# Kernel tuning notes

Measured on AMD Instinct MI355X. Metric: run time of the kernel, lower is better.

Reference implementation:

```python
import jax, jax.numpy as jnp
import numpy as np

IN_FEATURES = 4096
OUT_FEATURES = 4096


def fht(x):
    """Normalized fast Walsh-Hadamard transform along last axis (n = power of 2).
    Equals x @ H_n / sqrt(n); matches matmul_hadU(t)_cuda when had_K is None (K=1)."""
    n = x.shape[-1]
    orig_shape = x.shape
    x = x.reshape(-1, n)
    h = 1
    while h < n:
        x = x.reshape(-1, n // (2 * h), 2, h)
        a = x[:, :, 0, :]
        b = x[:, :, 1, :]
        x = jnp.stack([a + b, a - b], axis=2).reshape(-1, n)
        h *= 2
    scale = jnp.asarray(1.0 / np.sqrt(n), dtype=x.dtype)
    return (x * scale).reshape(orig_shape)


def decode_e8p(Qidxs, grid_abs):
    """E8P12-style decode: each 16-bit codeword -> 8 fp16 weights.
    Low 8 bits index a 256-entry table of 8 absolute values; high 8 bits are
    per-element sign flips. Returns dense W of shape [out, in]."""
    idx = Qidxs.astype(jnp.int32) & 0xFFFF            # [out, in/8]
    abs_vals = grid_abs[idx & 0xFF]                   # [out, in/8, 8]
    sbits = (idx[..., None] >> (8 + jnp.arange(8, dtype=jnp.int32))) & 1
    signs = (1 - 2 * sbits).astype(grid_abs.dtype)    # [out, in/8, 8] in {+1,-1}
    w = abs_vals * signs
    return w.reshape(Qidxs.shape[0], -1)              # [out, in]


def setup_inputs() -> dict:
    key = jax.random.key(0)
    k1, k2, k3, k4, k5, k6 = jax.random.split(key, 6)
    inp = {}
    inp["input"] = jax.random.normal(k1, (2, 4096, IN_FEATURES), dtype=jnp.float16)
    inp["Qidxs"] = jax.random.randint(k2, (OUT_FEATURES, IN_FEATURES // 8), 0, 65536, dtype=jnp.int32)
    # abs half-integer-ish grid values (E8 lattice magnitudes live in ~[0.25, 3.75])
    inp["grid_abs"] = (jax.random.uniform(k3, (256, 8), dtype=jnp.float32) * 3.0 + 0.25).astype(jnp.float16)
    # SU/SV are random sign vectors in QuIP
    inp["SU"] = (1 - 2 * jax.random.bernoulli(k4, 0.5, (IN_FEATURES,)).astype(jnp.float16))
    inp["SV"] = (1 - 2 * jax.random.bernoulli(k5, 0.5, (OUT_FEATURES,)).astype(jnp.float16))
    inp["Wscale"] = jnp.ones((), dtype=jnp.float32)
    inp["bias"] = jax.random.normal(k6, (OUT_FEATURES,), dtype=jnp.float16) * jnp.float16(0.01)
    return inp


def reference(input, Qidxs, grid_abs, SU, SV, Wscale, bias):
    x = input.reshape(-1, input.shape[-1])            # [T, in]
    x = x * SU                                        # input sign rescale
    x = fht(x)                                        # H^T x / sqrt(n) (H symmetric)
    x = (x * Wscale).astype(jnp.float16)              # global weight scale
    W = decode_e8p(Qidxs, grid_abs)                   # [out, in] dequantized lattice weights
    out = jnp.dot(x, W.T, preferred_element_type=jnp.float32).astype(jnp.float16)  # [T, out]
    out = fht(out)                                    # output Hadamard
    out = out * SV + bias                             # output sign rescale + bias
    return out.reshape(*input.shape[:-1], out.shape[-1])
```

## Files before the change

kernel.cpp:

```cpp
#include <hip/hip_runtime.h>
#include <hip/hip_bf16.h>
#include <stdint.h>

typedef _Float16 f16;
typedef _Float16 f16x8 __attribute__((ext_vector_type(8)));
typedef float f32x4 __attribute__((ext_vector_type(4)));

#define N_FEAT 4096
#define M_ROWS 8192
#define QSTRIDE 512

#define GLD16(gptr, lptr)                                                      \
  __builtin_amdgcn_global_load_lds(                                            \
      (const __attribute__((address_space(1))) void*)(gptr),                   \
      (__attribute__((address_space(3))) void*)(uint32_t)(uintptr_t)(lptr),    \
      16, 0, 0)

#define PAD64(i) ((i) + (((i) >> 6) << 2))

__device__ __forceinline__ void fht16(float v[16]) {
#pragma unroll
  for (int h = 1; h < 16; h <<= 1) {
#pragma unroll
    for (int i = 0; i < 16; i += (h << 1)) {
#pragma unroll
      for (int j = 0; j < h; ++j) {
        float a = v[i + j], b = v[i + j + h];
        v[i + j] = a + b;
        v[i + j + h] = a - b;
      }
    }
  }
}

__device__ __forceinline__ void fht4(float& a, float& b, float& c, float& d) {
  float t0 = a + b, t1 = a - b, t2 = c + d, t3 = c - d;
  a = t0 + t2; b = t1 + t3; c = t0 - t2; d = t1 - t3;
}

__global__ __launch_bounds__(256) void k_fht_in(const float* __restrict__ x,
                                                const float* __restrict__ SU,
                                                const float* __restrict__ wscale,
                                                f16* __restrict__ out) {
  __shared__ float lds[4096 + 256];
  const int row = blockIdx.x;
  const int t = threadIdx.x;
  const float* xr = x + (size_t)row * N_FEAT;
  float v[16];

#pragma unroll
  for (int j = 0; j < 4; ++j) {
    const float4 a = *(const float4*)(xr + (t << 4) + 4 * j);
    const float4 s = *(const float4*)(SU + (t << 4) + 4 * j);
    v[4 * j + 0] = a.x * s.x; v[4 * j + 1] = a.y * s.y;
    v[4 * j + 2] = a.z * s.z; v[4 * j + 3] = a.w * s.w;
  }
  fht16(v);
#pragma unroll
  for (int j = 0; j < 4; ++j)
    *(float4*)&lds[PAD64((t << 4) + 4 * j)] =
        make_float4(v[4 * j], v[4 * j + 1], v[4 * j + 2], v[4 * j + 3]);
  __syncthreads();

  const int a = t & 15, b = t >> 4;
#pragma unroll
  for (int j = 0; j < 16; ++j) v[j] = lds[PAD64((b << 8) + (j << 4) + a)];
  fht16(v);
#pragma unroll
  for (int j = 0; j < 16; ++j) lds[PAD64((b << 8) + (j << 4) + a)] = v[j];
  __syncthreads();

#pragma unroll
  for (int j = 0; j < 16; ++j) v[j] = lds[PAD64((j << 8) + t)];
  fht16(v);
  const float s = wscale[0] * 0.015625f;
  f16* op = out + (size_t)row * N_FEAT;
#pragma unroll
  for (int j = 0; j < 16; ++j) op[(j << 8) + t] = (f16)(v[j] * s);
}

__global__ __launch_bounds__(256) void k_wA(const int* __restrict__ q,
                                            const float* __restrict__ grid,
                                            f16* __restrict__ Wp) {
  __shared__ float tabf[2048];
  __shared__ float tile[64 * 65];
  const int t = threadIdx.x;
  const int kg = blockIdx.x;
  const int ng = blockIdx.y;
  {
    *(float4*)&tabf[t * 8] = *(const float4*)(grid + t * 8);
    *(float4*)&tabf[t * 8 + 4] = *(const float4*)(grid + t * 8 + 4);
  }
  __syncthreads();

#pragma unroll
  for (int e2 = 0; e2 < 2; ++e2) {
    const int e = t + (e2 << 8);
    const int nl = e >> 3, c = e & 7;
    const unsigned code =
        (unsigned)q[(size_t)(ng * 64 + nl) * QSTRIDE + kg * 8 + c] & 0xffffu;
    const float* tb = &tabf[(code & 255u) * 8];
#pragma unroll
    for (int j = 0; j < 8; ++j) {
      const int bi = __float_as_int(tb[j]) ^ (int)(((code >> (8 + j)) & 1u) << 31);
      tile[nl * 65 + (c << 3) + j] = __int_as_float(bi);
    }
  }
  __syncthreads();

  {
    const int k = t & 63, p = t >> 6;
    float v[16];
#pragma unroll
    for (int j = 0; j < 16; ++j) v[j] = tile[(16 * p + j) * 65 + k];
    fht16(v);
#pragma unroll
    for (int j = 0; j < 16; ++j) tile[(16 * p + j) * 65 + k] = v[j];
  }
  __syncthreads();

  {
    const int k = t & 63, base = (t >> 6) << 2;
#pragma unroll
    for (int bb = 0; bb < 4; ++bb) {
      const int low = base + bb;
      float v0 = tile[(low) * 65 + k],      v1 = tile[(low + 16) * 65 + k];
      float v2 = tile[(low + 32) * 65 + k], v3 = tile[(low + 48) * 65 + k];
      fht4(v0, v1, v2, v3);
      tile[(low) * 65 + k] = v0;      tile[(low + 16) * 65 + k] = v1;
      tile[(low + 32) * 65 + k] = v2; tile[(low + 48) * 65 + k] = v3;
    }
  }
  __syncthreads();

  {
    const int nl = t >> 2, koff = (t & 3) << 4;
    union { f16 h[16]; int4 v[2]; } u;
#pragma unroll
    for (int i = 0; i < 16; ++i) u.h[i] = (f16)tile[nl * 65 + koff + i];
    int4* dst = (int4*)(Wp + (size_t)(ng * 64 + nl) * N_FEAT + kg * 64 + koff);
    dst[0] = u.v[0];
    dst[1] = u.v[1];
  }
}

__global__ __launch_bounds__(256) void k_wB(f16* __restrict__ Wp) {
  __shared__ float tile[64 * 65];
  const int t = threadIdx.x;
  const int kg = blockIdx.x;
  const int n0 = blockIdx.y;
  {
    const int n1 = t >> 2, koff = (t & 3) << 4;
    const f16* src = Wp + (size_t)(n0 + 64 * n1) * N_FEAT + kg * 64 + koff;
    union { f16 h[16]; int4 v[2]; } u;
    u.v[0] = ((const int4*)src)[0];
    u.v[1] = ((const int4*)src)[1];
#pragma unroll
    for (int i = 0; i < 16; ++i) tile[n1 * 65 + koff + i] = (float)u.h[i];
  }
  __syncthreads();
  {
    const int k = t & 63, p = t >> 6;
    float v[16];
#pragma unroll
    for (int j = 0; j < 16; ++j) v[j] = tile[(16 * p + j) * 65 + k];
    fht16(v);
#pragma unroll
    for (int j = 0; j < 16; ++j) tile[(16 * p + j) * 65 + k] = v[j];
  }
  __syncthreads();
  {
    const int k = t & 63, base = (t >> 6) << 2;
#pragma unroll
    for (int bb = 0; bb < 4; ++bb) {
      const int low = base + bb;
      float v0 = tile[(low) * 65 + k],      v1 = tile[(low + 16) * 65 + k];
      float v2 = tile[(low + 32) * 65 + k], v3 = tile[(low + 48) * 65 + k];
      fht4(v0, v1, v2, v3);
      tile[(low) * 65 + k] = v0;      tile[(low + 16) * 65 + k] = v1;
      tile[(low + 32) * 65 + k] = v2; tile[(low + 48) * 65 + k] = v3;
    }
  }
  __syncthreads();
  {
    const int n1 = t >> 2, koff = (t & 3) << 4;
    union { f16 h[16]; int4 v[2]; } u;
#pragma unroll
    for (int i = 0; i < 16; ++i) u.h[i] = (f16)tile[n1 * 65 + koff + i];
    int4* dst = (int4*)(Wp + (size_t)(n0 + 64 * n1) * N_FEAT + kg * 64 + koff);
    dst[0] = u.v[0];
    dst[1] = u.v[1];
  }
}

#define BM 256
#define BN 256
#define BK 64
#define KDIM 4096

#define WAITB(n)                                          \
  asm volatile("s_waitcnt vmcnt(" #n ")" ::: "memory");   \
  __builtin_amdgcn_s_barrier();

#define SCHED_FENCE() __builtin_amdgcn_sched_barrier(0)

#define STAGE_HALF(gbase, lhalf)                                         \
  {                                                                      \
    _Pragma("unroll")                                                    \
    for (int i_ = 0; i_ < 2; ++i_) {                                     \
      const int rb_ = (w << 4) + (i_ << 3);                              \
      const int r_ = rb_ + srow;                                         \
      const int kc_ = scc ^ (r_ & 7);                                    \
      GLD16((gbase) + (size_t)r_ * KDIM + (kc_ << 3), (lhalf) + (rb_ << 6)); \
    }                                                                    \
  }

#define LDA(dst, mh)                                                     \
  {                                                                      \
    _Pragma("unroll")                                                    \
    for (int i_ = 0; i_ < 4; ++i_) {                                     \
      const int m_ = ((mh) << 7) + (wr << 6) + (i_ << 4) + ml;           \
      _Pragma("unroll")                                                  \
      for (int s_ = 0; s_ < 2; ++s_) {                                   \
        const int kc_ = ((s_ << 2) + quad) ^ (m_ & 7);                   \
        dst[i_][s_] = *(const f16x8*)&sA[cur][(m_ << 6) + (kc_ << 3)];   \
      }                                                                  \
    }                                                                    \
  }

#define LDB(dst, nh)                                                     \
  {                                                                      \
    _Pragma("unroll")                                                    \
    for (int j_ = 0; j_ < 2; ++j_) {                                     \
      const int n_ = ((nh) << 7) + (wc << 5) + (j_ << 4) + ml;           \
      _Pragma("unroll")                                                  \
      for (int s_ = 0; s_ < 2; ++s_) {                                   \
        const int kc_ = ((s_ << 2) + quad) ^ (n_ & 7);                   \
        dst[j_][s_] = *(const f16x8*)&sB[cur][(n_ << 6) + (kc_ << 3)];   \
      }                                                                  \
    }                                                                    \
  }

#define MMAQ(mh, nh)                                                     \
  {                                                                      \
    __builtin_amdgcn_s_setprio(1);                                       \
    _Pragma("unroll")                                                    \
    for (int i_ = 0; i_ < 4; ++i_) {                                     \
      _Pragma("unroll")                                                  \
      for (int j_ = 0; j_ < 2; ++j_) {                                   \
        acc[(mh) * 4 + i_][(nh) * 2 + j_] =                              \
            __builtin_amdgcn_mfma_f32_16x16x32_f16(                      \
                af[i_][0], bf[j_][0], acc[(mh) * 4 + i_][(nh) * 2 + j_], \
                0, 0, 0);                                                \
        acc[(mh) * 4 + i_][(nh) * 2 + j_] =                              \
            __builtin_amdgcn_mfma_f32_16x16x32_f16(                      \
                af[i_][1], bf[j_][1], acc[(mh) * 4 + i_][(nh) * 2 + j_], \
                0, 0, 0);                                                \
      }                                                                  \
    }                                                                    \
    __builtin_amdgcn_s_setprio(0);                                       \
  }

__global__ __launch_bounds__(512, 2) void k_gemm(const f16* __restrict__ A,
                                                 const f16* __restrict__ B,
                                                 float* __restrict__ C,
                                                 const float* __restrict__ SV,
                                                 const float* __restrict__ bias) {
  __shared__ __attribute__((aligned(16))) f16 sA[2][BM * BK];
  __shared__ __attribute__((aligned(16))) f16 sB[2][BN * BK];

  const int tid = threadIdx.x;
  const int lane = tid & 63;
  const int w = tid >> 6;
  const int wr = w >> 2;
  const int wc = w & 3;

  const int lin = blockIdx.y * gridDim.x + blockIdx.x;
  const int swz = ((lin & 7) << 6) | (lin >> 3);
  const int m0 = (swz >> 4) * BM;
  const int n0 = (swz & 15) * BN;

  const int quad = lane >> 4;
  const int ml = lane & 15;
  const int srow = lane >> 3;
  const int scc = lane & 7;

  f32x4 acc[8][4];
#pragma unroll
  for (int i = 0; i < 8; ++i)
#pragma unroll
    for (int j = 0; j < 4; ++j) acc[i][j] = (f32x4)0.0f;

  const f16* Ab = A + (size_t)m0 * KDIM;
  const f16* Bb = B + (size_t)n0 * KDIM;

  STAGE_HALF(Ab, &sA[0][0]);
  SCHED_FENCE();
  STAGE_HALF(Bb, &sB[0][0]);
  SCHED_FENCE();
  STAGE_HALF(Bb + (size_t)128 * KDIM, &sB[0][128 * 64]);
  SCHED_FENCE();
  STAGE_HALF(Ab + (size_t)128 * KDIM, &sA[0][128 * 64]);
  WAITB(4);

  f16x8 af[4][2], bf[2][2];

#pragma unroll 2
  for (int t = 0; t < 64; ++t) {
    const int cur = t & 1;
    const int nxt = cur ^ 1;
    const int kn = ((t + 1) & 63) << 6;
    const f16* An = Ab + kn;
    const f16* Bn = Bb + kn;

    STAGE_HALF(An, &sA[nxt][0]);
    LDA(af, 0);
    LDB(bf, 0);
    MMAQ(0, 0);

    WAITB(4);
    STAGE_HALF(Bn, &sB[nxt][0]);
    LDB(bf, 1);
    MMAQ(0, 1);

    WAITB(4);
    STAGE_HALF(Bn + (size_t)128 * KDIM, &sB[nxt][128 * 64]);
    LDA(af, 1);
    MMAQ(1, 1);

    SCHED_FENCE();
    STAGE_HALF(An + (size_t)128 * KDIM, &sA[nxt][128 * 64]);
    LDB(bf, 0);
    MMAQ(1, 0);
    WAITB(4);
  }

  asm volatile("s_waitcnt vmcnt(0)" ::: "memory");

#pragma unroll
  for (int nj = 0; nj < 4; ++nj) {
    const int col = n0 + ((nj >> 1) << 7) + (wc << 5) + ((nj & 1) << 4) + ml;
    const float sv = SV[col] * 0.015625f;
    const float bs = bias[col];
#pragma unroll
    for (int mi = 0; mi < 8; ++mi) {
      const int rowb =
          m0 + ((mi >> 2) << 7) + (wr << 6) + ((mi & 3) << 4) + (quad << 2);
#pragma unroll
      for (int r = 0; r < 4; ++r)
        C[(size_t)(rowb + r) * N_FEAT + col] = acc[mi][nj][r] * sv + bs;
    }
  }
}

extern "C" void kernel_launch(void* const* d_in, const int* in_sizes, int n_in,
                              void* d_out, int out_size, void* d_ws, size_t ws_size,
                              hipStream_t stream) {
  const float* input = nullptr;
  const int* qidxs = nullptr;
  const float* grid_abs = nullptr;
  const float* wscale = nullptr;
  const float* v4k[3] = {nullptr, nullptr, nullptr};
  int n4 = 0;
  for (int i = 0; i < n_in; ++i) {
    switch (in_sizes[i]) {
      case 33554432: input = (const float*)d_in[i]; break;
      case 2097152:  qidxs = (const int*)d_in[i]; break;
      case 2048:     grid_abs = (const float*)d_in[i]; break;
      case 1:        wscale = (const float*)d_in[i]; break;
      case 4096:     if (n4 < 3) v4k[n4++] = (const float*)d_in[i]; break;
      default: break;
    }
  }
  const float* SU = v4k[0];
  const float* SV = v4k[1];
  const float* bias = v4k[2];

  f16* x = (f16*)d_ws;
  f16* Wp;
  if (ws_size >= (size_t)100663296) {
    Wp = (f16*)((char*)d_ws + 67108864);
  } else {
    Wp = (f16*)const_cast<float*>(input);
  }
  float* out = (float*)d_out;

  k_fht_in<<<M_ROWS, 256, 0, stream>>>(input, SU, wscale, x);
  dim3 gw(64, 64);
  k_wA<<<gw, 256, 0, stream>>>(qidxs, grid_abs, Wp);
  k_wB<<<gw, 256, 0, stream>>>(Wp);
  dim3 g(N_FEAT / BN, M_ROWS / BM);
  k_gemm<<<g, 512, 0, stream>>>(x, Wp, out, SV, bias);
}
```

Baseline: 486.8 us.

## Restructure input FHT to one wavefront per row and keep both B fragments

The input Hadamard kernel now handles four rows per block, one wavefront per row, using an XOR-swizzled LDS layout and float4-vectorised LDS accesses in the second and third butterfly stages. Outputs are written as packed 4-wide f16 stores. In the GEMM, the low and high B fragments are held in separate registers, so the final quadrant reuses the low fragment instead of reloading it from LDS. This removes LDS traffic and bank conflicts at the cost of more VGPRs in the GEMM and larger LDS use per block in the FHT kernel.

```diff
diff --git a/kernel.cpp b/kernel.cpp
--- a/kernel.cpp
+++ b/kernel.cpp
@@ -33,50 +33,92 @@
   }
 }
 
+__device__ __forceinline__ void fht16v(f32x4 v[16]) {
+#pragma unroll
+  for (int h = 1; h < 16; h <<= 1) {
+#pragma unroll
+    for (int i = 0; i < 16; i += (h << 1)) {
+#pragma unroll
+      for (int j = 0; j < h; ++j) {
+        f32x4 a = v[i + j], b = v[i + j + h];
+        v[i + j] = a + b;
+        v[i + j + h] = a - b;
+      }
+    }
+  }
+}
+
 __device__ __forceinline__ void fht4(float& a, float& b, float& c, float& d) {
   float t0 = a + b, t1 = a - b, t2 = c + d, t3 = c - d;
   a = t0 + t2; b = t1 + t3; c = t0 - t2; d = t1 - t3;
 }
+
+#define SWZ(c) ((c) ^ (((((c) >> 4) ^ ((c) >> 8)) & 7) << 2))
 
 __global__ __launch_bounds__(256) void k_fht_in(const float* __restrict__ x,
                                                 const float* __restrict__ SU,
                                                 const float* __restrict__ wscale,
                                                 f16* __restrict__ out) {
-  __shared__ float lds[4096 + 256];
-  const int row = blockIdx.x;
+  __shared__ __attribute__((aligned(16))) float lds[4 * 4096];
   const int t = threadIdx.x;
-  const float* xr = x + (size_t)row * N_FEAT;
-  float v[16];
-
-#pragma unroll
-  for (int j = 0; j < 4; ++j) {
-    const float4 a = *(const float4*)(xr + (t << 4) + 4 * j);
-    const float4 s = *(const float4*)(SU + (t << 4) + 4 * j);
-    v[4 * j + 0] = a.x * s.x; v[4 * j + 1] = a.y * s.y;
-    v[4 * j + 2] = a.z * s.z; v[4 * j + 3] = a.w * s.w;
-  }
-  fht16(v);
-#pragma unroll
-  for (int j = 0; j < 4; ++j)
-    *(float4*)&lds[PAD64((t << 4) + 4 * j)] =
-        make_float4(v[4 * j], v[4 * j + 1], v[4 * j + 2], v[4 * j + 3]);
-  __syncthreads();
-
-  const int a = t & 15, b = t >> 4;
-#pragma unroll
-  for (int j = 0; j < 16; ++j) v[j] = lds[PAD64((b << 8) + (j << 4) + a)];
-  fht16(v);
-#pragma unroll
-  for (int j = 0; j < 16; ++j) lds[PAD64((b << 8) + (j << 4) + a)] = v[j];
-  __syncthreads();
-
-#pragma unroll
-  for (int j = 0; j < 16; ++j) v[j] = lds[PAD64((j << 8) + t)];
-  fht16(v);
-  const float s = wscale[0] * 0.015625f;
-  f16* op = out + (size_t)row * N_FEAT;
-#pragma unroll
-  for (int j = 0; j < 16; ++j) op[(j << 8) + t] = (f16)(v[j] * s);
+  const int rw = t >> 6;
+  const int u = t & 63;
+  const size_t row = (size_t)blockIdx.x * 4 + rw;
+  float* pl = &lds[rw << 12];
+  const float* xr = x + row * N_FEAT;
+
+#pragma unroll
+  for (int g = 0; g < 4; ++g) {
+    const int c16 = (g << 10) + (u << 4);
+    float v[16];
+#pragma unroll
+    for (int q = 0; q < 4; ++q) {
+      const f32x4 a = *(const f32x4*)(xr + c16 + (q << 2));
+      const f32x4 s4 = *(const f32x4*)(SU + c16 + (q << 2));
+      const f32x4 m = a * s4;
+      v[4 * q + 0] = m[0]; v[4 * q + 1] = m[1];
+      v[4 * q + 2] = m[2]; v[4 * q + 3] = m[3];
+    }
+    fht16(v);
+#pragma unroll
+    for (int q = 0; q < 4; ++q) {
+      const int col = c16 + (q << 2);
+      f32x4 wv = {v[4 * q + 0], v[4 * q + 1], v[4 * q + 2], v[4 * q + 3]};
+      *(f32x4*)&pl[SWZ(col)] = wv;
+    }
+  }
+  __syncthreads();
+
+  {
+    const int b = u >> 2, a4 = (u & 3) << 2;
+    f32x4 v[16];
+#pragma unroll
+    for (int jj = 0; jj < 16; ++jj)
+      v[jj] = *(const f32x4*)&pl[SWZ((b << 8) + (jj << 4) + a4)];
+    fht16v(v);
+#pragma unroll
+    for (int jj = 0; jj < 16; ++jj)
+      *(f32x4*)&pl[SWZ((b << 8) + (jj << 4) + a4)] = v[jj];
+  }
+  __syncthreads();
+
+  {
+    const int q4 = u << 2;
+    f32x4 v[16];
+#pragma unroll
+    for (int j = 0; j < 16; ++j)
+      v[j] = *(const f32x4*)&pl[SWZ((j << 8) + q4)];
+    fht16v(v);
+    const float s = wscale[0] * 0.015625f;
+    f16* op = out + row * N_FEAT;
+#pragma unroll
+    for (int j = 0; j < 16; ++j) {
+      union { f16 h[4]; uint2 u2; } pk;
+      pk.h[0] = (f16)(v[j][0] * s); pk.h[1] = (f16)(v[j][1] * s);
+      pk.h[2] = (f16)(v[j][2] * s); pk.h[3] = (f16)(v[j][3] * s);
+      *(uint2*)(op + (j << 8) + q4) = pk.u2;
+    }
+  }
 }
 
 __global__ __launch_bounds__(256) void k_wA(const int* __restrict__ q,
@@ -241,7 +283,7 @@
     }                                                                    \
   }
 
-#define MMAQ(mh, nh)                                                     \
+#define MMAQ(mh, nh, bfx)                                                \
   {                                                                      \
     __builtin_amdgcn_s_setprio(1);                                       \
     _Pragma("unroll")                                                    \
@@ -250,11 +292,11 @@
       for (int j_ = 0; j_ < 2; ++j_) {                                   \
         acc[(mh) * 4 + i_][(nh) * 2 + j_] =                              \
             __builtin_amdgcn_mfma_f32_16x16x32_f16(                      \
-                af[i_][0], bf[j_][0], acc[(mh) * 4 + i_][(nh) * 2 + j_], \
+                af[i_][0], bfx[j_][0], acc[(mh) * 4 + i_][(nh) * 2 + j_],\
                 0, 0, 0);                                                \
         acc[(mh) * 4 + i_][(nh) * 2 + j_] =                              \
             __builtin_amdgcn_mfma_f32_16x16x32_f16(                      \
-                af[i_][1], bf[j_][1], acc[(mh) * 4 + i_][(nh) * 2 + j_], \
+                af[i_][1], bfx[j_][1], acc[(mh) * 4 + i_][(nh) * 2 + j_],\
                 0, 0, 0);                                                \
       }                                                                  \
     }                                                                    \
@@ -303,7 +345,7 @@
   STAGE_HALF(Ab + (size_t)128 * KDIM, &sA[0][128 * 64]);
   WAITB(4);
 
-  f16x8 af[4][2], bf[2][2];
+  f16x8 af[4][2], bflo[2][2], bfhi[2][2];
 
 #pragma unroll 2
   for (int t = 0; t < 64; ++t) {
@@ -315,23 +357,22 @@
 
     STAGE_HALF(An, &sA[nxt][0]);
     LDA(af, 0);
-    LDB(bf, 0);
-    MMAQ(0, 0);
+    LDB(bflo, 0);
+    MMAQ(0, 0, bflo);
 
     WAITB(4);
     STAGE_HALF(Bn, &sB[nxt][0]);
-    LDB(bf, 1);
-    MMAQ(0, 1);
+    LDB(bfhi, 1);
+    MMAQ(0, 1, bfhi);
 
     WAITB(4);
     STAGE_HALF(Bn + (size_t)128 * KDIM, &sB[nxt][128 * 64]);
     LDA(af, 1);
-    MMAQ(1, 1);
+    MMAQ(1, 1, bfhi);
 
     SCHED_FENCE();
     STAGE_HALF(An + (size_t)128 * KDIM, &sA[nxt][128 * 64]);
-    LDB(bf, 0);
-    MMAQ(1, 0);
+    MMAQ(1, 0, bflo);
     WAITB(4);
   }
 
@@ -385,7 +426,7 @@
   }
   float* out = (float*)d_out;
 
-  k_fht_in<<<M_ROWS, 256, 0, stream>>>(input, SU, wscale, x);
+  k_fht_in<<<M_ROWS / 4, 256, 0, stream>>>(input, SU, wscale, x);
   dim3 gw(64, 64);
   k_wA<<<gw, 256, 0, stream>>>(qidxs, grid_abs, Wp);
   k_wB<<<gw, 256, 0, stream>>>(Wp);
```

After: 486.6 us. Within noise of the previous version (-0.0%).
